# Optimization experiments

Hardware: AMD Instinct MI355X
Metric: run time of the kernel (lower is better)

## Reference

```python
import jax, jax.numpy as jnp
import numpy as np

D = 128  # embedding dim (hardcoded by nn.Linear(128*2, 1))


def setup_inputs() -> dict:
    key = jax.random.key(0)
    k1, k2, k3, k4 = jax.random.split(key, 4)
    B, T, N = 256, 64, 2048
    targetsentence_emb = jax.random.normal(k1, (B, T, D), dtype=jnp.float32)
    context_emb = jax.random.normal(k2, (B, N, D), dtype=jnp.float32)
    # Linear(2D -> 1): weight [1, 2D], bias [1]. Store as flat vectors.
    W = jax.random.normal(k3, (2 * D,), dtype=jnp.float32) * (1.0 / np.sqrt(2 * D))
    b = jax.random.normal(k4, (1,), dtype=jnp.float32) * 0.01
    return {"targetsentence_emb": targetsentence_emb, "context_emb": context_emb, "W": W, "b": b}


def reference(targetsentence_emb, context_emb, W, b):
    # Decompose concat+Linear: W = [Wt | Wc], both length D.
    Wt, Wc = W[:D], W[D:]
    T = targetsentence_emb.shape[1]
    # score[b, n] = sum_t (Wt . target[b,t] + Wc . ctx[b,n] + bias)
    #            = sum_t(Wt . target[b,t]) + T * (Wc . ctx[b,n] + bias)
    tgt_term = jnp.einsum('btd,d->b', targetsentence_emb, Wt)  # [B]
    ctx_term = jnp.einsum('bnd,d->bn', context_emb, Wc)        # [B, N]
    scores = tgt_term[:, None] + T * (ctx_term + b[0])         # [B, N]
    attention = jax.nn.softmax(scores, axis=1)                 # softmax over context dim
    # einsum 'bnm,bnk->bnk' with m=1 is elementwise broadcast scaling
    return attention[:, :, None] * context_emb                 # [B, N, D]
```

## Files before the change

### kernel.cpp

```cpp
#include <hip/hip_runtime.h>


#define B_DIM 256
#define N_DIM 2048
#define D_DIM 128
#define DVEC  (D_DIM / 4)
#define T_SCALE 64.0f

typedef float f4v __attribute__((ext_vector_type(4)));

__global__ __launch_bounds__(256)
void k_scores(const float* __restrict__ ctx, const float* __restrict__ W,
              float* __restrict__ scores) {
    const int tid  = threadIdx.x;
    const int wave = tid >> 6;
    const int lane = tid & 63;
    const int sub  = lane & 31;
    const int half = lane >> 5;
    const int r    = blockIdx.x * 8 + wave * 2 + half;

    const float4 wc = ((const float4*)(W + D_DIM))[sub];
    const float4 v  = ((const float4*)ctx)[(size_t)r * DVEC + sub];
    float p = v.x * wc.x + v.y * wc.y + v.z * wc.z + v.w * wc.w;
    #pragma unroll
    for (int m = 1; m < 32; m <<= 1) p += __shfl_xor(p, m, 64);
    if (sub == 0) scores[r] = T_SCALE * p;
}

__global__ __launch_bounds__(256)
void k_softmax(float* __restrict__ s) {
    const int tid  = threadIdx.x;
    const int wave = tid >> 6;
    const int lane = tid & 63;
    float4* row4 = (float4*)(s + (size_t)blockIdx.x * N_DIM);

    __shared__ float red[4];

    float4 a = row4[tid];
    float4 c = row4[tid + 256];

    float m0 = fmaxf(fmaxf(fmaxf(a.x, a.y), fmaxf(a.z, a.w)),
                     fmaxf(fmaxf(c.x, c.y), fmaxf(c.z, c.w)));
    #pragma unroll
    for (int m = 1; m < 64; m <<= 1) m0 = fmaxf(m0, __shfl_xor(m0, m, 64));
    if (lane == 0) red[wave] = m0;
    __syncthreads();
    const float gmax = fmaxf(fmaxf(red[0], red[1]), fmaxf(red[2], red[3]));
    __syncthreads();

    a.x = __expf(a.x - gmax); a.y = __expf(a.y - gmax);
    a.z = __expf(a.z - gmax); a.w = __expf(a.w - gmax);
    c.x = __expf(c.x - gmax); c.y = __expf(c.y - gmax);
    c.z = __expf(c.z - gmax); c.w = __expf(c.w - gmax);

    float sum = a.x + a.y + a.z + a.w + c.x + c.y + c.z + c.w;
    #pragma unroll
    for (int m = 1; m < 64; m <<= 1) sum += __shfl_xor(sum, m, 64);
    if (lane == 0) red[wave] = sum;
    __syncthreads();
    const float inv = 1.0f / (red[0] + red[1] + red[2] + red[3]);

    a.x *= inv; a.y *= inv; a.z *= inv; a.w *= inv;
    c.x *= inv; c.y *= inv; c.z *= inv; c.w *= inv;
    row4[tid]       = a;
    row4[tid + 256] = c;
}

__global__ __launch_bounds__(256)
void k_scale(const float* __restrict__ ctx, const float* __restrict__ p,
             float* __restrict__ out) {
    const int tid = threadIdx.x;
    const int rb  = gridDim.x - 1 - blockIdx.x;
    const size_t base_row = (size_t)rb * 64;

    __shared__ float sp[64];
    if (tid < 64) sp[tid] = p[base_row + tid];
    __syncthreads();

    const f4v* c4 = (const f4v*)ctx + base_row * DVEC;
    f4v*       o4 = (f4v*)out       + base_row * DVEC;

    #pragma unroll
    for (int i = 0; i < 8; ++i) {
        const int f = i * 256 + tid;
        const float w = sp[f >> 5];
        f4v v = __builtin_nontemporal_load(&c4[f]);
        v *= w;
        __builtin_nontemporal_store(v, &o4[f]);
    }
}

extern "C" void kernel_launch(void* const* d_in, const int* in_sizes, int n_in,
                              void* d_out, int out_size, void* d_ws, size_t ws_size,
                              hipStream_t stream) {
    (void)in_sizes; (void)n_in; (void)out_size; (void)ws_size;
    const float* ctx = (const float*)d_in[1];
    const float* W   = (const float*)d_in[2];
    float* out       = (float*)d_out;
    float* scores    = (float*)d_ws;

    hipLaunchKernelGGL(k_scores,  dim3(B_DIM * N_DIM / 8), dim3(256), 0, stream,
                       ctx, W, scores);
    hipLaunchKernelGGL(k_softmax, dim3(B_DIM),             dim3(256), 0, stream,
                       scores);
    hipLaunchKernelGGL(k_scale,   dim3(B_DIM * N_DIM / 64), dim3(256), 0, stream,
                       ctx, scores, out);
}
```

Measured before the change: 467.5 us.

## Fuse score, softmax and scaling into one per-batch kernel

```diff
diff --git a/kernel.cpp b/kernel.cpp
--- a/kernel.cpp
+++ b/kernel.cpp
@@ -5,85 +5,73 @@
 #define N_DIM 2048
 #define D_DIM 128
 #define DVEC  (D_DIM / 4)
+#define NTHR  1024
 #define T_SCALE 64.0f
 
 typedef float f4v __attribute__((ext_vector_type(4)));
 
-__global__ __launch_bounds__(256)
-void k_scores(const float* __restrict__ ctx, const float* __restrict__ W,
-              float* __restrict__ scores) {
+__global__ __launch_bounds__(NTHR)
+void k_fused(const float* __restrict__ ctx, const float* __restrict__ W,
+             float* __restrict__ out) {
     const int tid  = threadIdx.x;
     const int wave = tid >> 6;
     const int lane = tid & 63;
     const int sub  = lane & 31;
     const int half = lane >> 5;
-    const int r    = blockIdx.x * 8 + wave * 2 + half;
+    const int b    = blockIdx.x;
 
-    const float4 wc = ((const float4*)(W + D_DIM))[sub];
-    const float4 v  = ((const float4*)ctx)[(size_t)r * DVEC + sub];
-    float p = v.x * wc.x + v.y * wc.y + v.z * wc.z + v.w * wc.w;
-    #pragma unroll
-    for (int m = 1; m < 32; m <<= 1) p += __shfl_xor(p, m, 64);
-    if (sub == 0) scores[r] = T_SCALE * p;
-}
+    __shared__ float sm[N_DIM];
+    __shared__ float red[16];
 
-__global__ __launch_bounds__(256)
-void k_softmax(float* __restrict__ s) {
-    const int tid  = threadIdx.x;
-    const int wave = tid >> 6;
-    const int lane = tid & 63;
-    float4* row4 = (float4*)(s + (size_t)blockIdx.x * N_DIM);
+    const size_t cbase = (size_t)b * ((size_t)N_DIM * DVEC);
+    const f4v* __restrict__ c4 = (const f4v*)ctx + cbase;
+    f4v*       __restrict__ o4 = (f4v*)out + cbase;
 
-    __shared__ float red[4];
+    const f4v wc = ((const f4v*)(W + D_DIM))[sub];
 
-    float4 a = row4[tid];
-    float4 c = row4[tid + 256];
-
-    float m0 = fmaxf(fmaxf(fmaxf(a.x, a.y), fmaxf(a.z, a.w)),
-                     fmaxf(fmaxf(c.x, c.y), fmaxf(c.z, c.w)));
-    #pragma unroll
-    for (int m = 1; m < 64; m <<= 1) m0 = fmaxf(m0, __shfl_xor(m0, m, 64));
-    if (lane == 0) red[wave] = m0;
-    __syncthreads();
-    const float gmax = fmaxf(fmaxf(red[0], red[1]), fmaxf(red[2], red[3]));
+    #pragma unroll 4
+    for (int it = 0; it < N_DIM / 32; ++it) {
+        const int n = it * 32 + wave * 2 + half;
+        const f4v v = c4[(size_t)n * DVEC + sub];
+        float p = v.x * wc.x + v.y * wc.y + v.z * wc.z + v.w * wc.w;
+        #pragma unroll
+        for (int m = 1; m < 32; m <<= 1) p += __shfl_xor(p, m, 64);
+        if (sub == 0) sm[n] = T_SCALE * p;
+    }
     __syncthreads();
 
-    a.x = __expf(a.x - gmax); a.y = __expf(a.y - gmax);
-    a.z = __expf(a.z - gmax); a.w = __expf(a.w - gmax);
-    c.x = __expf(c.x - gmax); c.y = __expf(c.y - gmax);
-    c.z = __expf(c.z - gmax); c.w = __expf(c.w - gmax);
+    const float a0 = sm[tid];
+    const float a1 = sm[tid + NTHR];
+    float mx = fmaxf(a0, a1);
+    #pragma unroll
+    for (int m = 1; m < 64; m <<= 1) mx = fmaxf(mx, __shfl_xor(mx, m, 64));
+    if (lane == 0) red[wave] = mx;
+    __syncthreads();
+    float gmax = red[0];
+    #pragma unroll
+    for (int i = 1; i < 16; ++i) gmax = fmaxf(gmax, red[i]);
 
-    float sum = a.x + a.y + a.z + a.w + c.x + c.y + c.z + c.w;
+    const float e0 = __expf(a0 - gmax);
+    const float e1 = __expf(a1 - gmax);
+    float s = e0 + e1;
     #pragma unroll
-    for (int m = 1; m < 64; m <<= 1) sum += __shfl_xor(sum, m, 64);
-    if (lane == 0) red[wave] = sum;
+    for (int m = 1; m < 64; m <<= 1) s += __shfl_xor(s, m, 64);
     __syncthreads();
-    const float inv = 1.0f / (red[0] + red[1] + red[2] + red[3]);
+    if (lane == 0) red[wave] = s;
+    __syncthreads();
+    float tot = red[0];
+    #pragma unroll
+    for (int i = 1; i < 16; ++i) tot += red[i];
+    const float inv = 1.0f / tot;
 
-    a.x *= inv; a.y *= inv; a.z *= inv; a.w *= inv;
-    c.x *= inv; c.y *= inv; c.z *= inv; c.w *= inv;
-    row4[tid]       = a;
-    row4[tid + 256] = c;
-}
-
-__global__ __launch_bounds__(256)
-void k_scale(const float* __restrict__ ctx, const float* __restrict__ p,
-             float* __restrict__ out) {
-    const int tid = threadIdx.x;
-    const int rb  = gridDim.x - 1 - blockIdx.x;
-    const size_t base_row = (size_t)rb * 64;
-
-    __shared__ float sp[64];
-    if (tid < 64) sp[tid] = p[base_row + tid];
+    sm[tid]        = e0 * inv;
+    sm[tid + NTHR] = e1 * inv;
     __syncthreads();
 
-    const f4v* c4 = (const f4v*)ctx + base_row * DVEC;
-    f4v*       o4 = (f4v*)out       + base_row * DVEC;
-
-    #pragma unroll
-    for (int i = 0; i < 8; ++i) {
-        const int f = i * 256 + tid;
-        const float w = sp[f >> 5];
+    #pragma unroll 4
+    for (int i = 0; i < (N_DIM * DVEC) / NTHR; ++i) {
+        const int f = i * NTHR + tid;
+        const float w = sm[f >> 5];
         f4v v = __builtin_nontemporal_load(&c4[f]);
         v *= w;
         __builtin_nontemporal_store(v, &o4[f]);
@@ -93,16 +81,11 @@
 extern "C" void kernel_launch(void* const* d_in, const int* in_sizes, int n_in,
                               void* d_out, int out_size, void* d_ws, size_t ws_size,
                               hipStream_t stream) {
-    (void)in_sizes; (void)n_in; (void)out_size; (void)ws_size;
+    (void)in_sizes; (void)n_in; (void)out_size; (void)d_ws; (void)ws_size;
     const float* ctx = (const float*)d_in[1];
     const float* W   = (const float*)d_in[2];
     float* out       = (float*)d_out;
-    float* scores    = (float*)d_ws;
 
-    hipLaunchKernelGGL(k_scores,  dim3(B_DIM * N_DIM / 8), dim3(256), 0, stream,
-                       ctx, W, scores);
-    hipLaunchKernelGGL(k_softmax, dim3(B_DIM),             dim3(256), 0, stream,
-                       scores);
-    hipLaunchKernelGGL(k_scale,   dim3(B_DIM * N_DIM / 64), dim3(256), 0, stream,
-                       ctx, scores, out);
+    hipLaunchKernelGGL(k_fused, dim3(B_DIM), dim3(NTHR), 0, stream,
+                       ctx, W, out);
 }
```

Result: no change. 473.6 us (+1.3%).
